# Optimization experiments

Hardware: AMD Instinct MI355X
Metric: run time of the kernel (lower is better)

Reference implementation:

```python
import jax, jax.numpy as jnp
import numpy as np

# --- model constants (match init_kwargs / Mamba2 defaults) ---
NUM_BLOCKS = 2
D_MODEL = 768
EXPAND = 2
D_INNER = EXPAND * D_MODEL          # 1536
D_STATE = 128
D_CONV = 4
HEADDIM = 64
NHEADS = D_INNER // HEADDIM         # 24
CONV_DIM = D_INNER + 2 * D_STATE    # 1792 (x, B, C go through the depthwise conv)
D_IN_PROJ = 2 * D_INNER + 2 * D_STATE + NHEADS  # 3352
VOCAB = 32000
LABEL_DIM = 1000
EPS = 1e-5


def _layernorm(x, w, b):
    mu = jnp.mean(x, axis=-1, keepdims=True)
    var = jnp.mean(jnp.square(x - mu), axis=-1, keepdims=True)
    return (x - mu) * jax.lax.rsqrt(var + EPS) * w + b


def _dwconv_causal(x, w, b):
    # x: [B, L, C], w: [C, K] depthwise kernel, b: [C]
    C, K = w.shape
    xt = jnp.transpose(x, (0, 2, 1))  # [B, C, L]
    out = jax.lax.conv_general_dilated(
        xt, w[:, None, :], window_strides=(1,), padding=[(K - 1, 0)],
        feature_group_count=C, dimension_numbers=("NCH", "OIH", "NCH"))
    return jnp.transpose(out, (0, 2, 1)) + b


def _ssd_scan(xh, Bm, Cm, dt, A):
    # xh: [B,L,H,P], Bm/Cm: [B,L,N], dt: [B,L,H], A: [H]
    Bsz, L, H, P = xh.shape
    N = Bm.shape[-1]
    dA = jnp.exp(dt * A)  # [B,L,H], in (0,1)

    def step(h, inp):
        xt, bt, ct, dat, dtt = inp  # [B,H,P],[B,N],[B,N],[B,H],[B,H]
        h = h * dat[:, :, None, None] + (dtt[:, :, None, None] * xt[..., None]) * bt[:, None, None, :]
        y = jnp.einsum('bhpn,bn->bhp', h, ct)
        return h, y

    h0 = jnp.zeros((Bsz, H, P, N), dtype=xh.dtype)
    xs = (jnp.transpose(xh, (1, 0, 2, 3)),
          jnp.transpose(Bm, (1, 0, 2)),
          jnp.transpose(Cm, (1, 0, 2)),
          jnp.transpose(dA, (1, 0, 2)),
          jnp.transpose(dt, (1, 0, 2)))
    _, ys = jax.lax.scan(step, h0, xs)  # ys: [L,B,H,P]
    return jnp.transpose(ys, (1, 0, 2, 3))


def _mamba2(x, Win, conv_w, conv_b, dt_bias, A_log, Dp, rms_w, Wout):
    Bsz, L, _ = x.shape
    zxbcdt = x @ Win  # [B,L,D_IN_PROJ]
    z = zxbcdt[..., :D_INNER]
    xBC = zxbcdt[..., D_INNER:D_INNER + CONV_DIM]
    dt = zxbcdt[..., D_INNER + CONV_DIM:]  # [B,L,H]
    dt = jax.nn.softplus(dt + dt_bias)

    xBC = jax.nn.silu(_dwconv_causal(xBC, conv_w, conv_b))
    xs = xBC[..., :D_INNER]
    Bm = xBC[..., D_INNER:D_INNER + D_STATE]
    Cm = xBC[..., D_INNER + D_STATE:]

    xh = xs.reshape(Bsz, L, NHEADS, HEADDIM)
    A = -jnp.exp(A_log)  # [H]
    y = _ssd_scan(xh, Bm, Cm, dt, A) + Dp[None, None, :, None] * xh  # [B,L,H,P]
    y = y.reshape(Bsz, L, D_INNER)

    # gated RMSNorm: norm(y * silu(z)) * weight
    y = y * jax.nn.silu(z)
    y = y * jax.lax.rsqrt(jnp.mean(jnp.square(y), axis=-1, keepdims=True) + EPS) * rms_w
    return y @ Wout


def _forward(tokens, emb, ln_w, ln_b, Win, conv_w, conv_b, dt_bias, A_log, Dp, rms_w, Wout, Wcls, bcls):
    x = emb[tokens]  # [B,L,D_MODEL]
    for i in range(NUM_BLOCKS):
        nx = _layernorm(x, ln_w[i], ln_b[i])
        x = x + _mamba2(nx, Win[i], conv_w[i], conv_b[i], dt_bias[i],
                        A_log[i], Dp[i], rms_w[i], Wout[i])
        # dropout_rate=0 (eval) -> identity; use_glu=False -> no post stage
    return x @ Wcls + bcls


def setup_inputs() -> dict:
    key = jax.random.key(0)
    ks = jax.random.split(key, 12)
    B, L = 2, 512
    tokens = jax.random.randint(ks[0], (B, L), 0, VOCAB)
    emb = jax.random.normal(ks[1], (VOCAB, D_MODEL), jnp.float32) * 0.02
    ln_w = jnp.ones((NUM_BLOCKS, D_MODEL), jnp.float32)
    ln_b = jnp.zeros((NUM_BLOCKS, D_MODEL), jnp.float32)
    Win = jax.random.normal(ks[2], (NUM_BLOCKS, D_MODEL, D_IN_PROJ), jnp.float32) / np.sqrt(D_MODEL)
    conv_w = jax.random.normal(ks[3], (NUM_BLOCKS, CONV_DIM, D_CONV), jnp.float32) / np.sqrt(D_CONV)
    conv_b = jnp.zeros((NUM_BLOCKS, CONV_DIM), jnp.float32)
    dt0 = jax.random.uniform(ks[4], (NUM_BLOCKS, NHEADS), jnp.float32, 1e-3, 0.1)
    dt_bias = dt0 + jnp.log(-jnp.expm1(-dt0))  # inverse softplus
    A_log = jnp.log(jax.random.uniform(ks[5], (NUM_BLOCKS, NHEADS), jnp.float32, 1.0, 16.0))
    Dp = jnp.ones((NUM_BLOCKS, NHEADS), jnp.float32)
    rms_w = jnp.ones((NUM_BLOCKS, D_INNER), jnp.float32)
    Wout = jax.random.normal(ks[6], (NUM_BLOCKS, D_INNER, D_MODEL), jnp.float32) / np.sqrt(D_INNER)
    Wcls = jax.random.normal(ks[7], (D_MODEL, LABEL_DIM), jnp.float32) / np.sqrt(D_MODEL)
    bcls = jnp.zeros((LABEL_DIM,), jnp.float32)
    return {"tokens": tokens, "emb": emb, "ln_w": ln_w, "ln_b": ln_b, "Win": Win,
            "conv_w": conv_w, "conv_b": conv_b, "dt_bias": dt_bias, "A_log": A_log,
            "Dp": Dp, "rms_w": rms_w, "Wout": Wout, "Wcls": Wcls, "bcls": bcls}


def reference(tokens, emb, ln_w, ln_b, Win, conv_w, conv_b, dt_bias, A_log, Dp, rms_w, Wout, Wcls, bcls):
    return _forward(tokens, emb, ln_w, ln_b, Win, conv_w, conv_b, dt_bias, A_log, Dp, rms_w, Wout, Wcls, bcls)
```

## Files before the change

kernel.cpp:

```cpp
#include <hip/hip_runtime.h>
#include <hip/hip_bf16.h>
#include <math.h>

#define B_SZ 2
#define L_SEQ 512
#define DMODEL 768
#define DINNER 1536
#define DSTATE 128
#define HEADDIM 64
#define NHEADS 24
#define CONVDIM 1792
#define DINPROJ 3352
#define ROWS (B_SZ * L_SEQ)

#define CHUNK 32
#define NCHUNK (L_SEQ / CHUNK)
#define BCDIM (2 * DSTATE)

#define NPAD_IN 3456
#define NPAD_CLS 1024

typedef __attribute__((ext_vector_type(8))) __bf16 bf16x8;
typedef __attribute__((ext_vector_type(4))) __bf16 bf16x4;
typedef __attribute__((ext_vector_type(4))) float f32x4;

typedef __attribute__((address_space(1))) const unsigned int as1_u32;
typedef __attribute__((address_space(3))) unsigned int as3_u32;

__device__ __forceinline__ void gload16(const void* g, void* s) {
  __builtin_amdgcn_global_load_lds((as1_u32*)(unsigned long)g, (as3_u32*)(unsigned long)s, 16, 0,
                                   0);
}

__device__ __forceinline__ float siluf(float x) { return x / (1.f + expf(-x)); }
__device__ __forceinline__ float softplusf(float x) {
  return x > 0.f ? x + log1pf(expf(-x)) : log1pf(expf(x));
}

__device__ __forceinline__ float block_reduce_sum(float v, float* sred) {
  int tid = threadIdx.x;
  for (int off = 32; off; off >>= 1) v += __shfl_down(v, off, 64);
  int wid = tid >> 6, lane = tid & 63;
  if (lane == 0) sred[wid] = v;
  __syncthreads();
  float total;
  if (tid == 0) {
    total = 0.f;
    int nw = blockDim.x >> 6;
    for (int i = 0; i < nw; ++i) total += sred[i];
    sred[0] = total;
  }
  __syncthreads();
  total = sred[0];
  __syncthreads();
  return total;
}

__global__ __launch_bounds__(256) void decomp_all_kernel(
    const float* __restrict__ Win, const float* __restrict__ Wout,
    const float* __restrict__ Wcls, const int* __restrict__ tok, const float* __restrict__ emb,
    const float* __restrict__ lnw0, const float* __restrict__ lnb0, float* __restrict__ x,
    __bf16* __restrict__ nxh, __bf16* __restrict__ nxl, __bf16* __restrict__ wih0,
    __bf16* __restrict__ wil0, __bf16* __restrict__ wih1, __bf16* __restrict__ wil1,
    __bf16* __restrict__ woh0, __bf16* __restrict__ wol0, __bf16* __restrict__ woh1,
    __bf16* __restrict__ wol1, __bf16* __restrict__ wch, __bf16* __restrict__ wcl) {
  constexpr int TIN = (NPAD_IN / 32) * (DMODEL / 32);
  constexpr int TOUT = (DMODEL / 32) * (DINNER / 32);
  constexpr int TCLS = (NPAD_CLS / 32) * (DMODEL / 32);
  __shared__ float tile[32][33];
  int bid = blockIdx.x;
  int tid = threadIdx.x;

  if (bid >= 2 * TIN + 2 * TOUT + TCLS) {
    int row = bid - (2 * TIN + 2 * TOUT + TCLS);
    int t = tok[row];
    float v[3];
    float s = 0.f;
#pragma unroll
    for (int j = 0; j < 3; ++j) {
      v[j] = emb[(size_t)t * DMODEL + tid + j * 256];
      s += v[j];
      x[(size_t)row * DMODEL + tid + j * 256] = v[j];
    }
    float* sred = (float*)tile;
    float mean = block_reduce_sum(s, sred) * (1.f / DMODEL);
    float s2 = 0.f;
#pragma unroll
    for (int j = 0; j < 3; ++j) {
      float d = v[j] - mean;
      s2 += d * d;
    }
    float var = block_reduce_sum(s2, sred) * (1.f / DMODEL);
    float r = 1.f / sqrtf(var + 1e-5f);
#pragma unroll
    for (int j = 0; j < 3; ++j) {
      int d = tid + j * 256;
      float val = (v[j] - mean) * r * lnw0[d] + lnb0[d];
      __bf16 h = (__bf16)val;
      nxh[(size_t)row * DMODEL + d] = h;
      nxl[(size_t)row * DMODEL + d] = (__bf16)(val - (float)h);
    }
    return;
  }

  const float* W;
  __bf16 *Th, *Tl;
  int K, N, ntx, r;
  if (bid < TIN) {
    W = Win; Th = wih0; Tl = wil0; K = DMODEL; N = DINPROJ; ntx = NPAD_IN / 32; r = bid;
  } else if (bid < 2 * TIN) {
    W = Win + (size_t)DMODEL * DINPROJ; Th = wih1; Tl = wil1; K = DMODEL; N = DINPROJ;
    ntx = NPAD_IN / 32; r = bid - TIN;
  } else if (bid < 2 * TIN + TOUT) {
    W = Wout; Th = woh0; Tl = wol0; K = DINNER; N = DMODEL; ntx = DMODEL / 32; r = bid - 2 * TIN;
  } else if (bid < 2 * TIN + 2 * TOUT) {
    W = Wout + (size_t)DINNER * DMODEL; Th = woh1; Tl = wol1; K = DINNER; N = DMODEL;
    ntx = DMODEL / 32; r = bid - 2 * TIN - TOUT;
  } else {
    W = Wcls; Th = wch; Tl = wcl; K = DMODEL; N = 1000; ntx = NPAD_CLS / 32;
    r = bid - 2 * TIN - 2 * TOUT;
  }
  int bn = (r % ntx) * 32, bk = (r / ntx) * 32;

  int i = tid >> 3, j4 = (tid & 7) * 4;
  int kk = bk + i;
  int nn = bn + j4;
  float4 v;
  if (nn + 3 < N) {
    v = *(const float4*)(W + (size_t)kk * N + nn);
  } else {
    v.x = (nn + 0 < N) ? W[(size_t)kk * N + nn + 0] : 0.f;
    v.y = (nn + 1 < N) ? W[(size_t)kk * N + nn + 1] : 0.f;
    v.z = (nn + 2 < N) ? W[(size_t)kk * N + nn + 2] : 0.f;
    v.w = (nn + 3 < N) ? W[(size_t)kk * N + nn + 3] : 0.f;
  }
  tile[i][j4 + 0] = v.x;
  tile[i][j4 + 1] = v.y;
  tile[i][j4 + 2] = v.z;
  tile[i][j4 + 3] = v.w;
  __syncthreads();
  int n = bn + i;
  bf16x4 hv, lv;
#pragma unroll
  for (int q = 0; q < 4; ++q) {
    float f = tile[j4 + q][i];
    __bf16 h = (__bf16)f;
    hv[q] = h;
    lv[q] = (__bf16)(f - (float)h);
  }
  *(bf16x4*)(Th + (size_t)n * K + bk + j4) = hv;
  *(bf16x4*)(Tl + (size_t)n * K + bk + j4) = lv;
}

__global__ __launch_bounds__(256) void ln_kernel(const float* __restrict__ x,
                                                 const float* __restrict__ w,
                                                 const float* __restrict__ b,
                                                 __bf16* __restrict__ oh,
                                                 __bf16* __restrict__ ol) {
  __shared__ float sred[8];
  int row = blockIdx.x, tid = threadIdx.x;
  const float* xr = x + (size_t)row * DMODEL;
  float v[3];
  float s = 0.f;
#pragma unroll
  for (int j = 0; j < 3; ++j) {
    v[j] = xr[tid + j * 256];
    s += v[j];
  }
  float mean = block_reduce_sum(s, sred) * (1.f / DMODEL);
  float s2 = 0.f;
#pragma unroll
  for (int j = 0; j < 3; ++j) {
    float d = v[j] - mean;
    s2 += d * d;
  }
  float var = block_reduce_sum(s2, sred) * (1.f / DMODEL);
  float r = 1.f / sqrtf(var + 1e-5f);
#pragma unroll
  for (int j = 0; j < 3; ++j) {
    int d = tid + j * 256;
    float val = (v[j] - mean) * r * w[d] + b[d];
    __bf16 h = (__bf16)val;
    oh[(size_t)row * DMODEL + d] = h;
    ol[(size_t)row * DMODEL + d] = (__bf16)(val - (float)h);
  }
}

__global__ __launch_bounds__(256) void act_decomp_kernel(const float* __restrict__ x,
                                                         __bf16* __restrict__ oh,
                                                         __bf16* __restrict__ ol) {
  int row = blockIdx.x, tid = threadIdx.x;
#pragma unroll
  for (int j = 0; j < 3; ++j) {
    int d = tid + j * 256;
    float v = x[(size_t)row * DMODEL + d];
    __bf16 h = (__bf16)v;
    oh[(size_t)row * DMODEL + d] = h;
    ol[(size_t)row * DMODEL + d] = (__bf16)(v - (float)h);
  }
}

template <int FM, int FN, bool ATOMIC>
__global__ __launch_bounds__(256) void mfma_gemm_kernel(
    const __bf16* __restrict__ Ahi, const __bf16* __restrict__ Alo,
    const __bf16* __restrict__ Bhi, const __bf16* __restrict__ Blo,
    const float* __restrict__ addsrc, const float* __restrict__ bias, float* __restrict__ C,
    int N, int K, int kslice, int nbx, int nby, int nwg) {
  constexpr int BM = FM * 32;
  constexpr int BN = FN * 32;
  constexpr int RGA = BM / 16;
  constexpr int RGB = BN / 16;
  constexpr int NITER = (2 * (RGA + RGB)) / 4;
  constexpr int ABYTES = BM * 64;
  constexpr int BBYTES = BN * 64;
  constexpr int BUFBYTES = 2 * ABYTES + 2 * BBYTES;
  __shared__ char lds[2 * BUFBYTES];

  int tid = threadIdx.x;
  int wave = tid >> 6, lane = tid & 63;
  int wm = wave >> 1, wn = wave & 1;
  int bx, by, kz;
  if (nbx > 0) {
    int orig = (blockIdx.x % 8) * (nwg / 8) + blockIdx.x / 8;
    bx = orig % nbx;
    int t = orig / nbx;
    if (nby > 0) {
      by = t % nby;
      kz = t / nby;
    } else {
      by = t;
      kz = 0;
    }
  } else {
    bx = blockIdx.x;
    by = blockIdx.y;
    kz = blockIdx.z;
  }
  int bm = by * BM;
  int bn = bx * BN;
  int kbeg = ATOMIC ? kz * kslice : 0;
  int kend = ATOMIC ? (kbeg + kslice) : K;
  int l2 = lane >> 2;
  int gch = (lane & 3) ^ ((lane >> 3) & 3);
  int lr = lane & 15, lg = lane >> 4;

  f32x4 acc[FM][FN] = {};

  auto stage = [&](char* buf, int k0) {
#pragma unroll
    for (int it = 0; it < NITER; ++it) {
      int rg = wave + it * 4;
      const __bf16* src;
      int row0, boff;
      if (rg < RGA) {
        src = Ahi;
        row0 = bm + rg * 16;
        boff = rg * 1024;
      } else if (rg < 2 * RGA) {
        src = Alo;
        row0 = bm + (rg - RGA) * 16;
        boff = ABYTES + (rg - RGA) * 1024;
      } else if (rg < 2 * RGA + RGB) {
        src = Bhi;
        row0 = bn + (rg - 2 * RGA) * 16;
        boff = 2 * ABYTES + (rg - 2 * RGA) * 1024;
      } else {
        src = Blo;
        row0 = bn + (rg - 2 * RGA - RGB) * 16;
        boff = 2 * ABYTES + BBYTES + (rg - 2 * RGA - RGB) * 1024;
      }
      gload16(src + (size_t)(row0 + l2) * K + k0 + gch * 8, buf + boff);
    }
  };

  stage(lds, kbeg);
  __syncthreads();

  char* curb = lds;
  char* nxtb = lds + BUFBYTES;
  for (int k0 = kbeg; k0 < kend; k0 += 32) {
    if (k0 + 32 < kend) stage(nxtb, k0 + 32);

    bf16x8 ahi[FM], alo[FM], bhi[FN], blo[FN];
#pragma unroll
    for (int m = 0; m < FM; ++m) {
      int r = wm * FM * 16 + m * 16 + lr;
      int off = r * 64 + ((lg ^ ((r >> 1) & 3)) * 16);
      ahi[m] = *(const bf16x8*)(curb + off);
      alo[m] = *(const bf16x8*)(curb + ABYTES + off);
    }
#pragma unroll
    for (int n = 0; n < FN; ++n) {
      int r = wn * FN * 16 + n * 16 + lr;
      int off = r * 64 + ((lg ^ ((r >> 1) & 3)) * 16);
      bhi[n] = *(const bf16x8*)(curb + 2 * ABYTES + off);
      blo[n] = *(const bf16x8*)(curb + 2 * ABYTES + BBYTES + off);
    }
#pragma unroll
    for (int m = 0; m < FM; ++m)
#pragma unroll
      for (int n = 0; n < FN; ++n) {
        acc[m][n] = __builtin_amdgcn_mfma_f32_16x16x32_bf16(ahi[m], bhi[n], acc[m][n], 0, 0, 0);
        acc[m][n] = __builtin_amdgcn_mfma_f32_16x16x32_bf16(ahi[m], blo[n], acc[m][n], 0, 0, 0);
        acc[m][n] = __builtin_amdgcn_mfma_f32_16x16x32_bf16(alo[m], bhi[n], acc[m][n], 0, 0, 0);
      }
    __syncthreads();
    char* t = curb;
    curb = nxtb;
    nxtb = t;
  }

#pragma unroll
  for (int m = 0; m < FM; ++m) {
#pragma unroll
    for (int n = 0; n < FN; ++n) {
      int gcol = bn + wn * FN * 16 + n * 16 + lr;
      if (gcol < N) {
#pragma unroll
        for (int r = 0; r < 4; ++r) {
          int grow = bm + wm * FM * 16 + m * 16 + lg * 4 + r;
          if (ATOMIC) {
            unsafeAtomicAdd(&C[(size_t)grow * N + gcol], acc[m][n][r]);
          } else {
            float v = acc[m][n][r];
            if (addsrc) v += addsrc[(size_t)grow * N + gcol];
            if (bias) v += bias[gcol];
            C[(size_t)grow * N + gcol] = v;
          }
        }
      }
    }
  }
}

__global__ __launch_bounds__(256) void convBC_kernel(const float* __restrict__ zx,
                                                     const float* __restrict__ cw,
                                                     const float* __restrict__ cb,
                                                     const float* __restrict__ dtb,
                                                     float* __restrict__ xBC,
                                                     float* __restrict__ dts) {
  int row = blockIdx.x;
  int c = threadIdx.x;
  int ch = DINNER + c;
  int l = row & (L_SEQ - 1);
  float acc = cb[ch];
#pragma unroll
  for (int k = 0; k < 4; ++k) {
    int ls = l - 3 + k;
    if (ls >= 0)
      acc = fmaf(cw[ch * 4 + k], zx[(size_t)(row - 3 + k) * DINPROJ + DINNER + ch], acc);
  }
  xBC[(size_t)row * BCDIM + c] = siluf(acc);
  if (c < NHEADS) {
    float raw = zx[(size_t)row * DINPROJ + DINNER + CONVDIM + c] + dtb[c];
    dts[(size_t)row * NHEADS + c] = softplusf(raw);
  }
}

__global__ __launch_bounds__(256) void sraw_kernel(const float* __restrict__ xBC,
                                                   float* __restrict__ Sraw) {
  __shared__ float Bs[CHUNK][132];
  __shared__ float Cs[CHUNK][132];
  int ci = blockIdx.x, b = blockIdx.y;
  int tid = threadIdx.x;
  int row0 = b * L_SEQ + ci * CHUNK;
#pragma unroll
  for (int i = 0; i < 4; ++i) {
    int vi = tid + i * 256;
    int t = vi >> 5;
    int n4 = (vi & 31) * 4;
    const float* r = xBC + (size_t)(row0 + t) * BCDIM;
    *(float4*)&Bs[t][n4] = *(const float4*)(r + n4);
    *(float4*)&Cs[t][n4] = *(const float4*)(r + DSTATE + n4);
  }
  __syncthreads();
  int t0 = (tid >> 4) * 2;
  int s0 = (tid & 15) * 2;
  float sacc[2][2] = {};
#pragma unroll
  for (int n = 0; n < DSTATE; n += 4) {
    float cr[2][4], br[2][4];
#pragma unroll
    for (int i = 0; i < 2; ++i) *(float4*)&cr[i][0] = *(const float4*)&Cs[t0 + i][n];
#pragma unroll
    for (int j = 0; j < 2; ++j) *(float4*)&br[j][0] = *(const float4*)&Bs[s0 + j][n];
#pragma unroll
    for (int i = 0; i < 2; ++i)
#pragma unroll
      for (int j = 0; j < 2; ++j)
#pragma unroll
        for (int k = 0; k < 4; ++k) sacc[i][j] = fmaf(cr[i][k], br[j][k], sacc[i][j]);
  }
  float* Sp = Sraw + ((size_t)(b * NCHUNK + ci) * CHUNK) * CHUNK;
#pragma unroll
  for (int i = 0; i < 2; ++i)
#pragma unroll
    for (int j = 0; j < 2; ++j) Sp[(t0 + i) * CHUNK + s0 + j] = sacc[i][j];
}

__global__ __launch_bounds__(256) void chunk_local_kernel(
    const float* __restrict__ zx, const float* __restrict__ xBC, const float* __restrict__ Sraw,
    const float* __restrict__ dts, const float* __restrict__ cw, const float* __restrict__ cb,
    const float* __restrict__ Alog, const float* __restrict__ Dp, float* __restrict__ y,
    __bf16* __restrict__ G, float* __restrict__ et, float* __restrict__ elast) {
  __shared__ float Bs[CHUNK][132];
  __shared__ float Xs[CHUNK][68];
  __shared__ float Ss[CHUNK][36];
  __shared__ float sP[CHUNK], sW[CHUNK], sDt[CHUNK];

  int ci = blockIdx.x, h = blockIdx.y, b = blockIdx.z;
  int bh = b * NHEADS + h;
  int tid = threadIdx.x;
  int row0 = b * L_SEQ + ci * CHUNK;

#pragma unroll
  for (int i = 0; i < 2; ++i) {
    int vi = tid + i * 256;
    int t = vi >> 4;
    int n8 = (vi & 15) * 8;
    const float* r = xBC + (size_t)(row0 + t) * BCDIM;
    *(float4*)&Bs[t][n8] = *(const float4*)(r + n8);
    *(float4*)&Bs[t][n8 + 4] = *(const float4*)(r + n8 + 4);
  }
#pragma unroll
  for (int i = 0; i < 2; ++i) {
    int vi = tid + i * 256;
    int t = vi >> 4;
    int p4 = (vi & 15) * 4;
    int cX = h * HEADDIM + p4;
    float oX[4];
#pragma unroll
    for (int q = 0; q < 4; ++q) oX[q] = cb[cX + q];
#pragma unroll
    for (int k = 0; k < 4; ++k) {
      if (ci > 0 || t + k >= 3) {
        float4 v = *(const float4*)(zx + (size_t)(row0 + t - 3 + k) * DINPROJ + DINNER + cX);
#pragma unroll
        for (int q = 0; q < 4; ++q) oX[q] = fmaf(cw[(cX + q) * 4 + k], ((const float*)&v)[q], oX[q]);
      }
    }
#pragma unroll
    for (int q = 0; q < 4; ++q) Xs[t][p4 + q] = siluf(oX[q]);
  }
  if (tid < 32) {
    int t = tid;
    float Ah = -expf(Alog[h]);
    float dtv = dts[(size_t)(row0 + t) * NHEADS + h];
    float P = dtv * Ah;
#pragma unroll
    for (int off = 1; off < 32; off <<= 1) {
      float u = __shfl_up(P, off, 32);
      if (t >= off) P += u;
    }
    float Plast = __shfl(P, 31, 32);
    float e = expf(P);
    sP[t] = P;
    sDt[t] = dtv;
    sW[t] = expf(Plast - P) * dtv;
    et[(size_t)(bh * NCHUNK + ci) * CHUNK + t] = e;
    if (t == 31) elast[bh * NCHUNK + ci] = e;
  }
  __syncthreads();

  int t0 = (tid >> 4) * 2;
  int s0 = (tid & 15) * 2;
  {
    const float* Sp = Sraw + ((size_t)(b * NCHUNK + ci) * CHUNK) * CHUNK;
#pragma unroll
    for (int i = 0; i < 2; ++i)
#pragma unroll
      for (int j = 0; j < 2; ++j) {
        int t = t0 + i, s = s0 + j;
        float sr = Sp[t * CHUNK + s];
        Ss[t][s] = (t >= s) ? sr * expf(sP[t] - sP[s]) * sDt[s] : 0.f;
      }
  }
  __syncthreads();

  {
    int p0 = (tid & 15) * 4;
    float acc[2][4] = {};
#pragma unroll
    for (int s = 0; s < CHUNK; s += 4) {
      float sr[2][4], xr[4][4];
#pragma unroll
      for (int i = 0; i < 2; ++i) *(float4*)&sr[i][0] = *(const float4*)&Ss[t0 + i][s];
#pragma unroll
      for (int u = 0; u < 4; ++u) *(float4*)&xr[u][0] = *(const float4*)&Xs[s + u][p0];
#pragma unroll
      for (int i = 0; i < 2; ++i)
#pragma unroll
        for (int j = 0; j < 4; ++j)
#pragma unroll
          for (int u = 0; u < 4; ++u) acc[i][j] = fmaf(sr[i][u], xr[u][j], acc[i][j]);
    }
    float Dh = Dp[h];
#pragma unroll
    for (int i = 0; i < 2; ++i) {
      int row = row0 + t0 + i;
      float4 o;
      o.x = acc[i][0] + Dh * Xs[t0 + i][p0 + 0];
      o.y = acc[i][1] + Dh * Xs[t0 + i][p0 + 1];
      o.z = acc[i][2] + Dh * Xs[t0 + i][p0 + 2];
      o.w = acc[i][3] + Dh * Xs[t0 + i][p0 + 3];
      *(float4*)(y + (size_t)row * DINNER + h * HEADDIM + p0) = o;
    }
  }

  {
    int n0 = (tid >> 4) * 8;
    int p0 = (tid & 15) * 4;
    float g[8][4] = {};
#pragma unroll 4
    for (int s = 0; s < CHUNK; ++s) {
      float w = sW[s];
      float bv[8], xv[4];
      *(float4*)&bv[0] = *(const float4*)&Bs[s][n0];
      *(float4*)&bv[4] = *(const float4*)&Bs[s][n0 + 4];
      *(float4*)&xv[0] = *(const float4*)&Xs[s][p0];
#pragma unroll
      for (int k = 0; k < 8; ++k) {
        float wb = w * bv[k];
#pragma unroll
        for (int j = 0; j < 4; ++j) g[k][j] = fmaf(wb, xv[j], g[k][j]);
      }
    }
    __bf16* Gp = G + ((size_t)bh * NCHUNK + ci) * (DSTATE * HEADDIM);
#pragma unroll
    for (int k = 0; k < 8; ++k) {
      bf16x4 o;
#pragma unroll
      for (int q = 0; q < 4; ++q) o[q] = (__bf16)g[k][q];
      *(bf16x4*)(Gp + (size_t)(n0 + k) * HEADDIM + p0) = o;
    }
  }
}

__global__ __launch_bounds__(256) void combine_kernel(__bf16* __restrict__ G,
                                                      const float* __restrict__ elast) {
  int part = blockIdx.x;
  int bh = blockIdx.y;
  int gi = part * 256 + threadIdx.x;
  __bf16* base = G + (size_t)bh * NCHUNK * (DSTATE * HEADDIM);
  const float* el = elast + bh * NCHUNK;
  float h0 = 0.f, h1 = 0.f, h2 = 0.f, h3 = 0.f;
#pragma unroll
  for (int c = 0; c < NCHUNK - 1; ++c) {
    bf16x4 g = *(bf16x4*)(base + (size_t)c * (DSTATE * HEADDIM) + gi * 4);
    float e = el[c];
    h0 = fmaf(e, h0, (float)g[0]);
    h1 = fmaf(e, h1, (float)g[1]);
    h2 = fmaf(e, h2, (float)g[2]);
    h3 = fmaf(e, h3, (float)g[3]);
    bf16x4 o;
    o[0] = (__bf16)h0;
    o[1] = (__bf16)h1;
    o[2] = (__bf16)h2;
    o[3] = (__bf16)h3;
    *(bf16x4*)(base + (size_t)c * (DSTATE * HEADDIM) + gi * 4) = o;
  }
}

__global__ __launch_bounds__(256) void apply_inter_kernel(const float* __restrict__ xBC,
                                                          const __bf16* __restrict__ G,
                                                          const float* __restrict__ et,
                                                          float* __restrict__ y) {
  __shared__ float Cs[CHUNK][132];
  __shared__ float Hs[DSTATE][68];
  __shared__ float sE[CHUNK];
  int ci = blockIdx.x + 1;
  int h = blockIdx.y, b = blockIdx.z;
  int bh = b * NHEADS + h;
  int tid = threadIdx.x;
  int row0 = b * L_SEQ + ci * CHUNK;

#pragma unroll
  for (int i = 0; i < 4; ++i) {
    int vi = tid + i * 256;
    int t = vi >> 5;
    int n4 = (vi & 31) * 4;
    *(float4*)&Cs[t][n4] = *(const float4*)(xBC + (size_t)(row0 + t) * BCDIM + DSTATE + n4);
  }
  const __bf16* Hsrc = G + ((size_t)bh * NCHUNK + (ci - 1)) * (DSTATE * HEADDIM);
#pragma unroll
  for (int i = 0; i < 8; ++i) {
    int vi = tid + i * 256;
    int n = vi >> 4;
    int p4 = (vi & 15) * 4;
    bf16x4 g = *(const bf16x4*)(Hsrc + (size_t)n * HEADDIM + p4);
#pragma unroll
    for (int q = 0; q < 4; ++q) Hs[n][p4 + q] = (float)g[q];
  }
  if (tid < CHUNK) sE[tid] = et[(size_t)(bh * NCHUNK + ci) * CHUNK + tid];
  __syncthreads();

  int t0 = (tid >> 4) * 2;
  int p0 = (tid & 15) * 4;
  float acc[2][4] = {};
#pragma unroll
  for (int n = 0; n < DSTATE; n += 4) {
    float cr[2][4], hr[4][4];
#pragma unroll
    for (int i = 0; i < 2; ++i) *(float4*)&cr[i][0] = *(const float4*)&Cs[t0 + i][n];
#pragma unroll
    for (int u = 0; u < 4; ++u) *(float4*)&hr[u][0] = *(const float4*)&Hs[n + u][p0];
#pragma unroll
    for (int i = 0; i < 2; ++i)
#pragma unroll
      for (int j = 0; j < 4; ++j)
#pragma unroll
        for (int u = 0; u < 4; ++u) acc[i][j] = fmaf(cr[i][u], hr[u][j], acc[i][j]);
  }
#pragma unroll
  for (int i = 0; i < 2; ++i) {
    int row = row0 + t0 + i;
    float e = sE[t0 + i];
    float* yp = y + (size_t)row * DINNER + h * HEADDIM + p0;
    float4 cur = *(float4*)yp;
    cur.x = fmaf(e, acc[i][0], cur.x);
    cur.y = fmaf(e, acc[i][1], cur.y);
    cur.z = fmaf(e, acc[i][2], cur.z);
    cur.w = fmaf(e, acc[i][3], cur.w);
    *(float4*)yp = cur;
  }
}

__global__ __launch_bounds__(256) void gate_rms_kernel(const float* __restrict__ y,
                                                       const float* __restrict__ zx,
                                                       const float* __restrict__ rmsw,
                                                       __bf16* __restrict__ oh,
                                                       __bf16* __restrict__ ol) {
  __shared__ float sred[8];
  int row = blockIdx.x, tid = threadIdx.x;
  const float* z = zx + (size_t)row * DINPROJ;
  const float* yr = y + (size_t)row * DINNER;
  float v[6];
  float ss = 0.f;
#pragma unroll
  for (int j = 0; j < 6; ++j) {
    int d = tid + j * 256;
    float val = yr[d] * siluf(z[d]);
    v[j] = val;
    ss += val * val;
  }
  float total = block_reduce_sum(ss, sred);
  float r = 1.f / sqrtf(total * (1.f / DINNER) + 1e-5f);
#pragma unroll
  for (int j = 0; j < 6; ++j) {
    int d = tid + j * 256;
    float val = v[j] * r * rmsw[d];
    __bf16 h = (__bf16)val;
    oh[(size_t)row * DINNER + d] = h;
    ol[(size_t)row * DINNER + d] = (__bf16)(val - (float)h);
  }
}

extern "C" void kernel_launch(void* const* d_in, const int* in_sizes, int n_in,
                              void* d_out, int out_size, void* d_ws, size_t ws_size,
                              hipStream_t stream) {
  const int* tokens = (const int*)d_in[0];
  const float* emb = (const float*)d_in[1];
  const float* ln_w = (const float*)d_in[2];
  const float* ln_b = (const float*)d_in[3];
  const float* Win = (const float*)d_in[4];
  const float* conv_w = (const float*)d_in[5];
  const float* conv_b = (const float*)d_in[6];
  const float* dt_bias = (const float*)d_in[7];
  const float* A_log = (const float*)d_in[8];
  const float* Dp = (const float*)d_in[9];
  const float* rms_w = (const float*)d_in[10];
  const float* Wout = (const float*)d_in[11];
  const float* Wcls = (const float*)d_in[12];
  const float* bcls = (const float*)d_in[13];
  float* out = (float*)d_out;

  float* ws = (float*)d_ws;
  float* x = ws;
  float* zx = x + (size_t)ROWS * DMODEL;
  float* y = zx + (size_t)ROWS * DINPROJ;
  __bf16* G = (__bf16*)(y + (size_t)ROWS * DINNER);
  float* et = (float*)(G + (size_t)B_SZ * NHEADS * NCHUNK * DSTATE * HEADDIM);
  float* elast = et + (size_t)B_SZ * NHEADS * NCHUNK * CHUNK;
  float* xBC = elast + B_SZ * NHEADS * NCHUNK;
  float* Sraw = xBC + (size_t)ROWS * BCDIM;
  float* dts = Sraw + (size_t)B_SZ * NCHUNK * CHUNK * CHUNK;
  __bf16* bp = (__bf16*)(dts + (size_t)ROWS * NHEADS);
  __bf16* nxh = bp;  bp += (size_t)ROWS * DMODEL;
  __bf16* nxl = bp;  bp += (size_t)ROWS * DMODEL;
  __bf16* yh = bp;   bp += (size_t)ROWS * DINNER;
  __bf16* yl = bp;   bp += (size_t)ROWS * DINNER;
  __bf16* xh = bp;   bp += (size_t)ROWS * DMODEL;
  __bf16* xl = bp;   bp += (size_t)ROWS * DMODEL;
  __bf16* wih0 = bp; bp += (size_t)NPAD_IN * DMODEL;
  __bf16* wil0 = bp; bp += (size_t)NPAD_IN * DMODEL;
  __bf16* wih1 = bp; bp += (size_t)NPAD_IN * DMODEL;
  __bf16* wil1 = bp; bp += (size_t)NPAD_IN * DMODEL;
  __bf16* woh0 = bp; bp += (size_t)DMODEL * DINNER;
  __bf16* wol0 = bp; bp += (size_t)DMODEL * DINNER;
  __bf16* woh1 = bp; bp += (size_t)DMODEL * DINNER;
  __bf16* wol1 = bp; bp += (size_t)DMODEL * DINNER;
  __bf16* wch = bp;  bp += (size_t)NPAD_CLS * DMODEL;
  __bf16* wcl = bp;

  constexpr int TIN = (NPAD_IN / 32) * (DMODEL / 32);
  constexpr int TOUT = (DMODEL / 32) * (DINNER / 32);
  constexpr int TCLS = (NPAD_CLS / 32) * (DMODEL / 32);
  decomp_all_kernel<<<2 * TIN + 2 * TOUT + TCLS + ROWS, 256, 0, stream>>>(
      Win, Wout, Wcls, tokens, emb, ln_w, ln_b, x, nxh, nxl, wih0, wil0, wih1, wil1, woh0, wol0,
      woh1, wol1, wch, wcl);

  for (int blk = 0; blk < 2; ++blk) {
    const float* cw_b = conv_w + (size_t)blk * CONVDIM * 4;
    const float* cb_b = conv_b + (size_t)blk * CONVDIM;
    const float* dtb_b = dt_bias + (size_t)blk * NHEADS;
    const float* Alog_b = A_log + (size_t)blk * NHEADS;
    const float* Dp_b = Dp + (size_t)blk * NHEADS;
    const float* rmsw_b = rms_w + (size_t)blk * DINNER;
    __bf16* wih = blk ? wih1 : wih0;
    __bf16* wil = blk ? wil1 : wil0;
    __bf16* woh = blk ? woh1 : woh0;
    __bf16* wol = blk ? wol1 : wol0;

    if (blk == 1) {
      ln_kernel<<<ROWS, 256, 0, stream>>>(x, ln_w + (size_t)blk * DMODEL,
                                          ln_b + (size_t)blk * DMODEL, nxh, nxl);
    }

    mfma_gemm_kernel<2, 2, false><<<(NPAD_IN / 64) * (ROWS / 64), 256, 0, stream>>>(
        nxh, nxl, wih, wil, nullptr, nullptr, zx, DINPROJ, DMODEL, 0, NPAD_IN / 64, 0,
        (NPAD_IN / 64) * (ROWS / 64));

    convBC_kernel<<<ROWS, BCDIM, 0, stream>>>(zx, cw_b, cb_b, dtb_b, xBC, dts);

    sraw_kernel<<<dim3(NCHUNK, B_SZ), 256, 0, stream>>>(xBC, Sraw);

    chunk_local_kernel<<<dim3(NCHUNK, NHEADS, B_SZ), 256, 0, stream>>>(
        zx, xBC, Sraw, dts, cw_b, cb_b, Alog_b, Dp_b, y, G, et, elast);

    combine_kernel<<<dim3(8, B_SZ * NHEADS), 256, 0, stream>>>(G, elast);

    apply_inter_kernel<<<dim3(NCHUNK - 1, NHEADS, B_SZ), 256, 0, stream>>>(xBC, G, et, y);

    gate_rms_kernel<<<ROWS, 256, 0, stream>>>(y, zx, rmsw_b, yh, yl);

    mfma_gemm_kernel<2, 2, true><<<(DMODEL / 64) * (ROWS / 64) * 4, 256, 0, stream>>>(
        yh, yl, woh, wol, nullptr, nullptr, x, DMODEL, DINNER, DINNER / 4, DMODEL / 64,
        ROWS / 64, (DMODEL / 64) * (ROWS / 64) * 4);
  }

  act_decomp_kernel<<<ROWS, 256, 0, stream>>>(x, xh, xl);
  mfma_gemm_kernel<2, 2, false><<<(NPAD_CLS / 64) * (ROWS / 64), 256, 0, stream>>>(
      xh, xl, wch, wcl, nullptr, bcls, out, 1000, DMODEL, 0, NPAD_CLS / 64, 0,
      (NPAD_CLS / 64) * (ROWS / 64));
}
```

Baseline: 248.2 us.

## Use bf16 MFMA for inter-chunk state apply with transposed swizzled state layout

The chunk state G is now stored transposed (p-major, n contiguous) with an XOR swizzle on 8-element groups. apply_inter_kernel loads it straight into LDS with gload16 and converts C to bf16 in swizzled LDS. The C·H product is then computed with 16x16x32 bf16 MFMA instructions instead of scalar FP32 FMAs. The elementwise combine kernel does not depend on layout, so it keeps working. This cuts FP32 ALU work and LDS traffic but drops C to bf16 precision, and y is updated with scalar rather than float4 read-modify-writes.

Measured after the change: 240.0 us. -3.3%, faster.

```diff
diff --git a/kernel.cpp b/kernel.cpp
--- a/kernel.cpp
+++ b/kernel.cpp
@@ -402,7 +402,7 @@
     const float* __restrict__ zx, const float* __restrict__ xBC, const float* __restrict__ Sraw,
     const float* __restrict__ dts, const float* __restrict__ cw, const float* __restrict__ cb,
     const float* __restrict__ Alog, const float* __restrict__ Dp, float* __restrict__ y,
-    __bf16* __restrict__ G, float* __restrict__ et, float* __restrict__ elast) {
+    __bf16* __restrict__ Gt, float* __restrict__ et, float* __restrict__ elast) {
   __shared__ float Bs[CHUNK][132];
   __shared__ float Xs[CHUNK][68];
   __shared__ float Ss[CHUNK][36];
@@ -525,13 +525,16 @@
         for (int j = 0; j < 4; ++j) g[k][j] = fmaf(wb, xv[j], g[k][j]);
       }
     }
-    __bf16* Gp = G + ((size_t)bh * NCHUNK + ci) * (DSTATE * HEADDIM);
-#pragma unroll
-    for (int k = 0; k < 8; ++k) {
-      bf16x4 o;
-#pragma unroll
-      for (int q = 0; q < 4; ++q) o[q] = (__bf16)g[k][q];
-      *(bf16x4*)(Gp + (size_t)(n0 + k) * HEADDIM + p0) = o;
+    __bf16* Gp = Gt + ((size_t)bh * NCHUNK + ci) * (DSTATE * HEADDIM);
+    int cchunk = tid >> 4;
+#pragma unroll
+    for (int j = 0; j < 4; ++j) {
+      int p = p0 + j;
+      int cs = cchunk ^ (p & 7);
+      bf16x8 o;
+#pragma unroll
+      for (int k = 0; k < 8; ++k) o[k] = (__bf16)g[k][j];
+      *(bf16x8*)(Gp + (size_t)p * DSTATE + cs * 8) = o;
     }
   }
 }
@@ -562,66 +565,67 @@
 }
 
 __global__ __launch_bounds__(256) void apply_inter_kernel(const float* __restrict__ xBC,
-                                                          const __bf16* __restrict__ G,
+                                                          const __bf16* __restrict__ Gt,
                                                           const float* __restrict__ et,
                                                           float* __restrict__ y) {
-  __shared__ float Cs[CHUNK][132];
-  __shared__ float Hs[DSTATE][68];
+  __shared__ __bf16 CsB[CHUNK * DSTATE];
+  __shared__ __bf16 HsB[HEADDIM * DSTATE];
   __shared__ float sE[CHUNK];
   int ci = blockIdx.x + 1;
   int h = blockIdx.y, b = blockIdx.z;
   int bh = b * NHEADS + h;
   int tid = threadIdx.x;
+  int wave = tid >> 6, lane = tid & 63;
   int row0 = b * L_SEQ + ci * CHUNK;
 
-#pragma unroll
-  for (int i = 0; i < 4; ++i) {
+  const __bf16* Hsrc = Gt + ((size_t)bh * NCHUNK + (ci - 1)) * (DSTATE * HEADDIM);
+#pragma unroll
+  for (int r = 0; r < 4; ++r) {
+    gload16(Hsrc + (size_t)r * 2048 + wave * 512 + lane * 8,
+            (char*)HsB + r * 4096 + wave * 1024);
+  }
+#pragma unroll
+  for (int i = 0; i < 2; ++i) {
     int vi = tid + i * 256;
-    int t = vi >> 5;
-    int n4 = (vi & 31) * 4;
-    *(float4*)&Cs[t][n4] = *(const float4*)(xBC + (size_t)(row0 + t) * BCDIM + DSTATE + n4);
-  }
-  const __bf16* Hsrc = G + ((size_t)bh * NCHUNK + (ci - 1)) * (DSTATE * HEADDIM);
-#pragma unroll
-  for (int i = 0; i < 8; ++i) {
-    int vi = tid + i * 256;
-    int n = vi >> 4;
-    int p4 = (vi & 15) * 4;
-    bf16x4 g = *(const bf16x4*)(Hsrc + (size_t)n * HEADDIM + p4);
-#pragma unroll
-    for (int q = 0; q < 4; ++q) Hs[n][p4 + q] = (float)g[q];
+    int t = vi >> 4;
+    int c = vi & 15;
+    const float* src = xBC + (size_t)(row0 + t) * BCDIM + DSTATE + c * 8;
+    float4 v0 = *(const float4*)src;
+    float4 v1 = *(const float4*)(src + 4);
+    bf16x8 o;
+    o[0] = (__bf16)v0.x; o[1] = (__bf16)v0.y; o[2] = (__bf16)v0.z; o[3] = (__bf16)v0.w;
+    o[4] = (__bf16)v1.x; o[5] = (__bf16)v1.y; o[6] = (__bf16)v1.z; o[7] = (__bf16)v1.w;
+    int cs = c ^ (t & 7);
+    *(bf16x8*)&CsB[t * DSTATE + cs * 8] = o;
   }
   if (tid < CHUNK) sE[tid] = et[(size_t)(bh * NCHUNK + ci) * CHUNK + tid];
   __syncthreads();
 
-  int t0 = (tid >> 4) * 2;
-  int p0 = (tid & 15) * 4;
-  float acc[2][4] = {};
-#pragma unroll
-  for (int n = 0; n < DSTATE; n += 4) {
-    float cr[2][4], hr[4][4];
-#pragma unroll
-    for (int i = 0; i < 2; ++i) *(float4*)&cr[i][0] = *(const float4*)&Cs[t0 + i][n];
-#pragma unroll
-    for (int u = 0; u < 4; ++u) *(float4*)&hr[u][0] = *(const float4*)&Hs[n + u][p0];
-#pragma unroll
-    for (int i = 0; i < 2; ++i)
-#pragma unroll
-      for (int j = 0; j < 4; ++j)
-#pragma unroll
-        for (int u = 0; u < 4; ++u) acc[i][j] = fmaf(cr[i][u], hr[u][j], acc[i][j]);
-  }
-#pragma unroll
-  for (int i = 0; i < 2; ++i) {
-    int row = row0 + t0 + i;
-    float e = sE[t0 + i];
-    float* yp = y + (size_t)row * DINNER + h * HEADDIM + p0;
-    float4 cur = *(float4*)yp;
-    cur.x = fmaf(e, acc[i][0], cur.x);
-    cur.y = fmaf(e, acc[i][1], cur.y);
-    cur.z = fmaf(e, acc[i][2], cur.z);
-    cur.w = fmaf(e, acc[i][3], cur.w);
-    *(float4*)yp = cur;
+  int lr = lane & 15, lg = lane >> 4;
+  int wm = wave >> 1;
+  int wnb = (wave & 1) * 2;
+  f32x4 acc[2] = {};
+#pragma unroll
+  for (int ks = 0; ks < 4; ++ks) {
+    int ar = wm * 16 + lr;
+    bf16x8 af = *(const bf16x8*)&CsB[ar * DSTATE + (((ks * 4 + lg) ^ (ar & 7)) * 8)];
+#pragma unroll
+    for (int nn = 0; nn < 2; ++nn) {
+      int br = (wnb + nn) * 16 + lr;
+      bf16x8 bfr = *(const bf16x8*)&HsB[br * DSTATE + (((ks * 4 + lg) ^ (br & 7)) * 8)];
+      acc[nn] = __builtin_amdgcn_mfma_f32_16x16x32_bf16(af, bfr, acc[nn], 0, 0, 0);
+    }
+  }
+#pragma unroll
+  for (int nn = 0; nn < 2; ++nn) {
+    int p = (wnb + nn) * 16 + lr;
+#pragma unroll
+    for (int r = 0; r < 4; ++r) {
+      int t = wm * 16 + lg * 4 + r;
+      float e = sE[t];
+      float* yp = &y[(size_t)(row0 + t) * DINNER + h * HEADDIM + p];
+      *yp = fmaf(e, acc[nn][r], *yp);
+    }
   }
 }
 
@@ -678,8 +682,8 @@
   float* x = ws;
   float* zx = x + (size_t)ROWS * DMODEL;
   float* y = zx + (size_t)ROWS * DINPROJ;
-  __bf16* G = (__bf16*)(y + (size_t)ROWS * DINNER);
-  float* et = (float*)(G + (size_t)B_SZ * NHEADS * NCHUNK * DSTATE * HEADDIM);
+  __bf16* Gt = (__bf16*)(y + (size_t)ROWS * DINNER);
+  float* et = (float*)(Gt + (size_t)B_SZ * NHEADS * NCHUNK * DSTATE * HEADDIM);
   float* elast = et + (size_t)B_SZ * NHEADS * NCHUNK * CHUNK;
   float* xBC = elast + B_SZ * NHEADS * NCHUNK;
   float* Sraw = xBC + (size_t)ROWS * BCDIM;
@@ -735,11 +739,11 @@
     sraw_kernel<<<dim3(NCHUNK, B_SZ), 256, 0, stream>>>(xBC, Sraw);
 
     chunk_local_kernel<<<dim3(NCHUNK, NHEADS, B_SZ), 256, 0, stream>>>(
-        zx, xBC, Sraw, dts, cw_b, cb_b, Alog_b, Dp_b, y, G, et, elast);
-
-    combine_kernel<<<dim3(8, B_SZ * NHEADS), 256, 0, stream>>>(G, elast);
-
-    apply_inter_kernel<<<dim3(NCHUNK - 1, NHEADS, B_SZ), 256, 0, stream>>>(xBC, G, et, y);
+        zx, xBC, Sraw, dts, cw_b, cb_b, Alog_b, Dp_b, y, Gt, et, elast);
+
+    combine_kernel<<<dim3(8, B_SZ * NHEADS), 256, 0, stream>>>(Gt, elast);
+
+    apply_inter_kernel<<<dim3(NCHUNK - 1, NHEADS, B_SZ), 256, 0, stream>>>(xBC, Gt, et, y);
 
     gate_rms_kernel<<<ROWS, 256, 0, stream>>>(y, zx, rmsw_b, yh, yl);
 
```
